# Kernel optimization log

Measured on AMD Instinct MI355X. Metric: run time of the kernel, lower is better.

Reference implementation:

```python
import jax, jax.numpy as jnp
import numpy as np

N_NODES = 16000
N_EDGES = 512000
N_TYPES = 87      # atomic numbers covered by gfn2-xtb embedding
EMBED_DIM = 28    # 16s + 8p + 4d aux basis size
NODE_DIM = 128
NUM_BASIS = 20
CUTOFF = 5.0
P_ORDER = 5       # polynomial cutoff order
MUL0, MUL1, MUL2 = 128, 64, 32  # multiplicities of 0e, 1e, 2e irreps


def setup_inputs() -> dict:
    key = jax.random.key(0)
    k1, k2, k3, k4, k5, k6 = jax.random.split(key, 6)
    at_no = jax.random.randint(k1, (N_NODES,), 1, N_TYPES)
    # spread atoms so edge distances cover (0, cutoff] and beyond
    pos = jax.random.normal(k2, (N_NODES, 3), dtype=jnp.float32) * 3.0
    src = jax.random.randint(k3, (N_EDGES,), 0, N_NODES)
    off = jax.random.randint(k4, (N_EDGES,), 1, N_NODES)  # guarantee src != dst (no zero dist)
    dst = (src + off) % N_NODES
    edge_index = jnp.stack([src, dst])
    embed_table = jax.random.normal(k5, (N_TYPES, EMBED_DIM), dtype=jnp.float32)
    W = jax.random.normal(k6, (NODE_DIM, EMBED_DIM), dtype=jnp.float32) / np.float32(np.sqrt(EMBED_DIM))
    b = jnp.zeros((NODE_DIM,), dtype=jnp.float32)  # nn.init.zeros_(bias)
    return {"at_no": at_no, "pos": pos, "edge_index": edge_index,
            "embed_table": embed_table, "W": W, "b": b}


def _sph_harm_lmax2(u):
    """e3nn real spherical harmonics l=0,1,2, normalize=True (u is unit), 'component' norm."""
    x, y, z = u[..., 0], u[..., 1], u[..., 2]
    sh0 = jnp.ones_like(x)[..., None]                       # [E,1]
    s3 = np.float32(np.sqrt(3.0))
    sh1 = s3 * u                                            # [E,3]
    s15 = np.float32(np.sqrt(15.0))
    s5 = np.float32(np.sqrt(5.0))
    sh2 = jnp.stack([
        s15 * x * z,
        s15 * x * y,
        s5 * (y * y - 0.5 * (x * x + z * z)),
        s15 * y * z,
        0.5 * s15 * (z * z - x * x),
    ], axis=-1)                                             # [E,5]
    return sh0, sh1, sh2


def reference(at_no, pos, edge_index, embed_table, W, b):
    pos = pos[:, jnp.array([1, 2, 0])]                      # axis permutation from forward()
    vec = pos[edge_index[0]] - pos[edge_index[1]]           # [E,3] edge gather
    dist = jnp.linalg.norm(vec, axis=-1, keepdims=True)     # [E,1]

    # scalar node features: Int2c1e embedding lookup + Linear
    x_scalar = embed_table[at_no] @ W.T + b                 # [N,128]

    # Bessel RBF: sqrt(2/c) * sin(n*pi*d/c) / d, n = 1..num_basis
    n = jnp.arange(1, NUM_BASIS + 1, dtype=pos.dtype)
    rbf = np.float32(np.sqrt(2.0 / CUTOFF)) * jnp.sin(n * jnp.pi * dist / CUTOFF) / dist  # [E,20]

    # polynomial cutoff (DimeNet-style, order p)
    u = dist / CUTOFF
    p = float(P_ORDER)
    ca = -(p + 1.0) * (p + 2.0) / 2.0
    cb = p * (p + 2.0)
    cc = -p * (p + 1.0) / 2.0
    fcut = jnp.where(u < 1.0,
                     1.0 + ca * u ** P_ORDER + cb * u ** (P_ORDER + 1) + cc * u ** (P_ORDER + 2),
                     0.0)                                   # [E,1]

    # real spherical harmonics on unit edge vectors, tiled per irrep multiplicity
    unit = vec / dist
    sh0, sh1, sh2 = _sph_harm_lmax2(unit)
    rsh = jnp.concatenate([jnp.tile(sh0, (1, MUL0)),
                           jnp.tile(sh1, (1, MUL1)),
                           jnp.tile(sh2, (1, MUL2))], axis=-1)  # [E, 480]

    return x_scalar, rbf, fcut, rsh
```

## Files before the change

kernel.cpp:

```cpp
#include <hip/hip_runtime.h>
#include <math.h>

#define N_NODES   16000
#define N_EDGES   512000
#define EMBED_DIM 28
#define NODE_DIM  128
#define NUM_BASIS 20

#define EPB   128
#define NBLK  (N_EDGES / EPB)

#define PSTRIDE 516
#define PAT_DWORDS (8 * PSTRIDE + EPB * 4)

typedef float f32x4 __attribute__((ext_vector_type(4)));

__global__ __launch_bounds__(256) void node_kernel(
    const int*   __restrict__ at_no,
    const float* __restrict__ embed,
    const float* __restrict__ W,
    const float* __restrict__ b,
    float*       __restrict__ out)
{
    int idx = blockIdx.x * 256 + threadIdx.x;
    if (idx >= N_NODES * NODE_DIM) return;
    int node = idx >> 7;
    int d    = idx & 127;
    int a    = at_no[node];
    const float* er = embed + a * EMBED_DIM;
    const float* wr = W + d * EMBED_DIM;
    float sum = b[d];
#pragma unroll
    for (int k = 0; k < EMBED_DIM; ++k)
        sum = fmaf(er[k], wr[k], sum);
    out[idx] = sum;
}

__global__ __launch_bounds__(128) void fused_edge_kernel(
    const float* __restrict__ pos,
    const int*   __restrict__ eidx,
    float*       __restrict__ rbf,
    float*       __restrict__ fcut,
    float*       __restrict__ rsh)
{
    __shared__ float sh_pat[PAT_DWORDS];
    __shared__ float sh_rbf[EPB * 20];

    const int t  = threadIdx.x;
    const int e0 = blockIdx.x * EPB;
    const int e  = e0 + t;

    {
        int s  = eidx[e];
        int dn = eidx[N_EDGES + e];

        float ax = pos[s*3+1],  ay = pos[s*3+2],  az = pos[s*3+0];
        float bx = pos[dn*3+1], by = pos[dn*3+2], bz = pos[dn*3+0];
        float vx = ax - bx, vy = ay - by, vz = az - bz;
        float dist = sqrtf(vx*vx + vy*vy + vz*vz);
        float inv  = 1.0f / dist;
        float ux = vx*inv, uy = vy*inv, uz = vz*inv;

        const float S3  = 1.7320508075688772f;
        const float S5  = 2.2360679774997896f;
        const float S15 = 3.8729833462074170f;
        float s0 = S3 * ux, s1 = S3 * uy, s2 = S3 * uz;
        float t0 = S15 * ux * uz;
        float t1 = S15 * ux * uy;
        float t2 = S5  * (uy*uy - 0.5f*(ux*ux + uz*uz));
        float t3 = S15 * uy * uz;
        float t4 = 0.5f * S15 * (uz*uz - ux*ux);

        f32x4* pb = (f32x4*)(sh_pat) + t;
#define PW(j, a_, b_, c_, d_) { f32x4 v_; v_.x=a_; v_.y=b_; v_.z=c_; v_.w=d_; \
                                pb[(j) * (PSTRIDE/4)] = v_; }
        PW(0, 1.0f, 1.0f, 1.0f, 1.0f)
        PW(1, s0, s1, s2, s0)
        PW(2, s1, s2, s0, s1)
        PW(3, s2, s0, s1, s2)
        PW(4, t0, t1, t2, t3)
        PW(5, t1, t2, t3, t4)
        PW(6, t2, t3, t4, t0)
        PW(7, t3, t4, t0, t1)
        PW(8, t4, t0, t1, t2)
#undef PW

        float u  = dist * 0.2f;
        float u2 = u*u, u5 = u2*u2*u;
        float f  = 1.0f + u5*(-21.0f + u*(35.0f - 15.0f*u));
        fcut[e] = (u < 1.0f) ? f : 0.0f;

        float th = 0.62831853071795864769f * dist;
        float sn = __sinf(th), cs = __cosf(th);
        float twoc = 2.0f * cs;
        float kk = 0.6324555320336759f * inv;
        float sp = 0.0f, sc = sn;
        f32x4* rb = (f32x4*)(sh_rbf + t * 20);
#pragma unroll
        for (int q = 0; q < 5; ++q) {
            f32x4 v_;
            v_.x = kk * sc; { float nx = twoc*sc - sp; sp = sc; sc = nx; }
            v_.y = kk * sc; { float nx = twoc*sc - sp; sp = sc; sc = nx; }
            v_.z = kk * sc; { float nx = twoc*sc - sp; sp = sc; sc = nx; }
            v_.w = kk * sc; { float nx = twoc*sc - sp; sp = sc; sc = nx; }
            rb[q] = v_;
        }
    }
    __syncthreads();

    {
        const f32x4* ls = (const f32x4*)sh_rbf;
        f32x4* go = (f32x4*)(rbf + (size_t)e0 * NUM_BASIS);
#pragma unroll
        for (int q = 0; q < 5; ++q)
            go[q * EPB + t] = ls[q * EPB + t];
    }

    {
        int offs[15];
#pragma unroll
        for (int k = 0; k < 15; ++k) {
            int u  = k * 128 + t;
            int d  = u / 120;
            int c  = u - d * 120;
            int p;
            if (c < 32)      p = 0;
            else if (c < 80) p = 1 + (c - 32) % 3;
            else             p = 4 + (4 * (c - 80)) % 5;
            offs[k] = p * PSTRIDE + d * 4;
        }

        float* outb = rsh + (size_t)e0 * 480 + (size_t)t * 4;
        int base = 0;

#pragma unroll 1
        for (int i = 0; i < 8; ++i) {
#pragma unroll
            for (int k = 0; k < 15; ++k) {
                f32x4 v = *(const f32x4*)(sh_pat + base + offs[k]);
                *(f32x4*)(outb + (size_t)k * 512) = v;
            }
            base += 64;
            outb += 15 * 512;
        }
    }
}

extern "C" void kernel_launch(void* const* d_in, const int* in_sizes, int n_in,
                              void* d_out, int out_size, void* d_ws, size_t ws_size,
                              hipStream_t stream) {
    const int*   at_no = (const int*)  d_in[0];
    const float* pos   = (const float*)d_in[1];
    const int*   eidx  = (const int*)  d_in[2];
    const float* embed = (const float*)d_in[3];
    const float* W     = (const float*)d_in[4];
    const float* b     = (const float*)d_in[5];

    float* out      = (float*)d_out;
    float* x_scalar = out;
    float* rbf      = x_scalar + (size_t)N_NODES * NODE_DIM;
    float* fcut     = rbf + (size_t)N_EDGES * NUM_BASIS;
    float* rsh      = fcut + N_EDGES;

    node_kernel<<<(N_NODES * NODE_DIM + 255) / 256, 256, 0, stream>>>(
        at_no, embed, W, b, x_scalar);

    fused_edge_kernel<<<NBLK, 128, 0, stream>>>(
        pos, eidx, rbf, fcut, rsh);
}
```

Before: 217.2 us.

## Merge node embedding kernel into edge kernel and store RBF directly to global

Folds the node-feature linear layer into the edge kernel as extra trailing blocks, so a single launch covers both and the launch gap and tail of the first kernel go away. Each node block handles 8 nodes. The RBF values are also written straight from registers to global memory instead of being staged through shared memory for coalesced stores. This saves LDS and a copy pass, but each thread now writes a contiguous 80-byte row, so the global writes are less coalesced.

```diff
diff --git a/kernel.cpp b/kernel.cpp
--- a/kernel.cpp
+++ b/kernel.cpp
@@ -10,43 +10,49 @@
 #define EPB   128
 #define NBLK  (N_EDGES / EPB)
 
+#define NODE_BLOCKS 2000
+#define NODE_CHUNKS 8
+
 #define PSTRIDE 516
 #define PAT_DWORDS (8 * PSTRIDE + EPB * 4)
 
 typedef float f32x4 __attribute__((ext_vector_type(4)));
 
-__global__ __launch_bounds__(256) void node_kernel(
+__global__ __launch_bounds__(128) void fused_all_kernel(
     const int*   __restrict__ at_no,
+    const float* __restrict__ pos,
+    const int*   __restrict__ eidx,
     const float* __restrict__ embed,
     const float* __restrict__ W,
-    const float* __restrict__ b,
-    float*       __restrict__ out)
-{
-    int idx = blockIdx.x * 256 + threadIdx.x;
-    if (idx >= N_NODES * NODE_DIM) return;
-    int node = idx >> 7;
-    int d    = idx & 127;
-    int a    = at_no[node];
-    const float* er = embed + a * EMBED_DIM;
-    const float* wr = W + d * EMBED_DIM;
-    float sum = b[d];
-#pragma unroll
-    for (int k = 0; k < EMBED_DIM; ++k)
-        sum = fmaf(er[k], wr[k], sum);
-    out[idx] = sum;
-}
-
-__global__ __launch_bounds__(128) void fused_edge_kernel(
-    const float* __restrict__ pos,
-    const int*   __restrict__ eidx,
+    const float* __restrict__ bias,
+    float*       __restrict__ x_scalar,
     float*       __restrict__ rbf,
     float*       __restrict__ fcut,
     float*       __restrict__ rsh)
 {
+    const int t = threadIdx.x;
+
+    if (blockIdx.x >= NBLK) {
+        int bid2 = blockIdx.x - NBLK;
+#pragma unroll 1
+        for (int ch = 0; ch < NODE_CHUNKS; ++ch) {
+            int idx  = (bid2 * NODE_CHUNKS + ch) * 128 + t;
+            int node = idx >> 7;
+            int d    = idx & 127;
+            int a    = at_no[node];
+            const float* er = embed + a * EMBED_DIM;
+            const float* wr = W + d * EMBED_DIM;
+            float sum = bias[d];
+#pragma unroll
+            for (int k = 0; k < EMBED_DIM; ++k)
+                sum = fmaf(er[k], wr[k], sum);
+            x_scalar[idx] = sum;
+        }
+        return;
+    }
+
     __shared__ float sh_pat[PAT_DWORDS];
-    __shared__ float sh_rbf[EPB * 20];
 
-    const int t  = threadIdx.x;
     const int e0 = blockIdx.x * EPB;
     const int e  = e0 + t;
 
@@ -95,7 +101,7 @@
         float twoc = 2.0f * cs;
         float kk = 0.6324555320336759f * inv;
         float sp = 0.0f, sc = sn;
-        f32x4* rb = (f32x4*)(sh_rbf + t * 20);
+        f32x4* rb = (f32x4*)(rbf + (size_t)e * NUM_BASIS);
 #pragma unroll
         for (int q = 0; q < 5; ++q) {
             f32x4 v_;
@@ -107,14 +113,6 @@
         }
     }
     __syncthreads();
-
-    {
-        const f32x4* ls = (const f32x4*)sh_rbf;
-        f32x4* go = (f32x4*)(rbf + (size_t)e0 * NUM_BASIS);
-#pragma unroll
-        for (int q = 0; q < 5; ++q)
-            go[q * EPB + t] = ls[q * EPB + t];
-    }
 
     {
         int offs[15];
@@ -162,9 +160,6 @@
     float* fcut     = rbf + (size_t)N_EDGES * NUM_BASIS;
     float* rsh      = fcut + N_EDGES;
 
-    node_kernel<<<(N_NODES * NODE_DIM + 255) / 256, 256, 0, stream>>>(
-        at_no, embed, W, b, x_scalar);
-
-    fused_edge_kernel<<<NBLK, 128, 0, stream>>>(
-        pos, eidx, rbf, fcut, rsh);
+    fused_all_kernel<<<NBLK + NODE_BLOCKS, 128, 0, stream>>>(
+        at_no, pos, eidx, embed, W, b, x_scalar, rbf, fcut, rsh);
 }
```

Measured after the change: 229.0 us. 1.05x slower.
